# Kernel optimization log

Measured on AMD Instinct MI355X. Metric: run time of the kernel, lower is better.

Reference implementation:

```python
import jax, jax.numpy as jnp
import numpy as np
from jax.scipy.special import logsumexp

T, B, D, L = 1024, 32, 768, 48
NEG = jnp.float32(-1e20)


def setup_inputs() -> dict:
    key = jax.random.key(0)
    ks = jax.random.split(key, 10)
    feats = jax.random.normal(ks[0], (T, B, D), jnp.float32)
    # tags: True = label disallowed at this position (partial annotation mask)
    tags = jax.random.uniform(ks[1], (T, B, L)) < 0.3
    lens = jax.random.randint(ks[2], (B,), T // 2, T + 1)
    W = jax.random.normal(ks[3], (D, L), jnp.float32) * 0.02
    b = jnp.zeros((L,), jnp.float32)
    base = jnp.float32(1.0 / L)
    begin_transition = jnp.full((L,), base) + 0.01 * jax.random.normal(ks[4], (L,), jnp.float32)
    transitions = jnp.full((L, L), base) + 0.01 * jax.random.normal(ks[5], (L, L), jnp.float32)
    end_transition = jnp.full((L,), base) + 0.01 * jax.random.normal(ks[6], (L,), jnp.float32)
    begin_constraints = jax.random.uniform(ks[7], (L,)) < 0.2
    end_constraints = jax.random.uniform(ks[8], (L,)) < 0.2
    transition_constraints = jax.random.uniform(ks[9], (L, L)) < 0.2
    return {
        "feats": feats, "tags": tags, "lens": lens,
        "W": W, "b": b,
        "begin_transition": begin_transition, "transitions": transitions,
        "end_transition": end_transition,
        "begin_constraints": begin_constraints, "end_constraints": end_constraints,
        "transition_constraints": transition_constraints,
    }


def _crf_logZ(emissions, begin, trans, end, tag_mask, lens):
    """Forward algorithm over [T,B,L] emissions; tag_mask True = disallowed.
    Returns log partition per batch element, read out at step lens-1."""
    fs0 = emissions[0] + begin[None, :]              # [B, L]
    fs0 = jnp.where(tag_mask[0], NEG, fs0)

    def step(prev, xs):
        em_t, m_t = xs
        # new[b, j] = logsumexp_k(prev[b, k] + trans[j, k]) + em_t[b, j]
        new = logsumexp(prev[:, None, :] + trans[None, :, :], axis=-1) + em_t
        new = jnp.where(m_t, NEG, new)
        return new, new

    _, ys = jax.lax.scan(step, fs0, (emissions[1:], tag_mask[1:]))
    all_fs = jnp.concatenate([fs0[None], ys], axis=0)        # [T, B, L]
    last = all_fs[lens - 1, jnp.arange(lens.shape[0])]       # [B, L]
    return logsumexp(last + end[None, :], axis=-1)           # [B]


def reference(feats, tags, lens, W, b, begin_transition, transitions,
              end_transition, begin_constraints, end_constraints,
              transition_constraints):
    # feature2labels (Dropout is identity in eval)
    emissions = jnp.einsum('tbd,dl->tbl', feats, W) + b      # [T, B, L]
    no_mask = jnp.zeros_like(tags)

    # forward_alg: unconstrained partition function
    fwd = _crf_logZ(emissions, begin_transition, transitions,
                    end_transition, no_mask, lens)

    # partial_score: constrained params + gold tag masking
    begin_m = jnp.where(begin_constraints, NEG, begin_transition)
    trans_m = jnp.where(transition_constraints, NEG, transitions)
    end_m = jnp.where(end_constraints, NEG, end_transition)
    par = _crf_logZ(emissions, begin_m, trans_m, end_m, tags, lens)

    # criterion per batch element (sum over batch = original scalar loss)
    return fwd - par                                          # [B]
```

## Files before the change

kernel.cpp:

```cpp
#include <hip/hip_runtime.h>

#define T_ 1024
#define B_ 32
#define D_ 768
#define L_ 48
#define TB_ (T_ * B_)

typedef __attribute__((ext_vector_type(4))) float f32x4;

__global__ __launch_bounds__(256, 2) void emis_gemm(
    const float* __restrict__ feats, const float* __restrict__ W,
    const float* __restrict__ bias, float* __restrict__ E) {
  __shared__ float fbuf[64 * 64];
  __shared__ float wbuf[48 * 68];
  const int tid = threadIdx.x;
  const int wv = tid >> 6;
  const int lane = tid & 63;
  const int cg = tid & 7;
  const int rg = tid >> 3;
  const int c0 = cg * 6;
  const int rowbase = blockIdx.x * 64;
  const int r7 = rg & 7;
  const int r_in = lane >> 4;
  const int slot = lane & 15;

  float acc[2][6];
#pragma unroll
  for (int i = 0; i < 2; i++)
#pragma unroll
    for (int c = 0; c < 6; c++) acc[i][c] = 0.f;

  for (int kc = 0; kc < D_; kc += 64) {
    __syncthreads();

#pragma unroll
    for (int inst = 0; inst < 4; inst++) {
      const int rowstart = wv * 16 + inst * 4;
      const int r = rowstart + r_in;
      const int gch = slot ^ (r & 7);
      const float* g = feats + (size_t)(rowbase + r) * D_ + kc + gch * 4;
      float* l = fbuf + rowstart * 64;
      __builtin_amdgcn_global_load_lds(
          (const __attribute__((address_space(1))) uint32_t*)g,
          (__attribute__((address_space(3))) uint32_t*)l, 16, 0, 0);
    }

#pragma unroll
    for (int i = 0; i < 12; i++) {
      const int idx = tid + i * 256;
      const int ko = idx / 48;
      const int j = idx - ko * 48;
      wbuf[j * 68 + ko] = W[(kc + ko) * L_ + j];
    }

    __syncthreads();

#pragma unroll 4
    for (int k4 = 0; k4 < 16; k4++) {
      float4 fv[2];
      float4 wv4[6];
      const int sch = (k4 ^ r7) << 2;
#pragma unroll
      for (int i = 0; i < 2; i++)
        fv[i] = *(const float4*)(fbuf + (rg + 32 * i) * 64 + sch);
#pragma unroll
      for (int cc = 0; cc < 6; cc++)
        wv4[cc] = *(const float4*)(wbuf + (c0 + cc) * 68 + k4 * 4);
#pragma unroll
      for (int i = 0; i < 2; i++) {
#pragma unroll
        for (int cc = 0; cc < 6; cc++) {
          acc[i][cc] = fmaf(fv[i].x, wv4[cc].x, acc[i][cc]);
          acc[i][cc] = fmaf(fv[i].y, wv4[cc].y, acc[i][cc]);
          acc[i][cc] = fmaf(fv[i].z, wv4[cc].z, acc[i][cc]);
          acc[i][cc] = fmaf(fv[i].w, wv4[cc].w, acc[i][cc]);
        }
      }
    }
  }

#pragma unroll
  for (int i = 0; i < 2; i++) {
    float* dst = E + (size_t)(rowbase + rg + 32 * i) * L_ + c0;
#pragma unroll
    for (int cc = 0; cc < 6; cc += 2) {
      float2 v;
      v.x = __expf(acc[i][cc + 0] + bias[c0 + cc + 0]);
      v.y = __expf(acc[i][cc + 1] + bias[c0 + cc + 1]);
      *(float2*)(dst + cc) = v;
    }
  }
}

__global__ __launch_bounds__(128) void crf_scan(
    const float* __restrict__ E, const int* __restrict__ tags,
    const int* __restrict__ lens, const float* __restrict__ begin,
    const float* __restrict__ trans, const float* __restrict__ endt,
    const int* __restrict__ bc, const int* __restrict__ ec,
    const int* __restrict__ tc, float* __restrict__ out) {
  __shared__ __align__(16) float sbuf[2][2][64];
  __shared__ __align__(16) float pbuf[2][48 * 52];
  __shared__ float lzbuf[2];
  const int b = blockIdx.x;
  const int wv = threadIdx.x >> 6;
  const int lane = threadIdx.x & 63;
  const bool act = lane < L_;
  const bool par = (wv == 1);
  const int len = lens[b];
  const int stride = B_ * L_;
  const int base = b * L_ + (act ? lane : 0);

  if (act) {
#pragma unroll
    for (int k = 0; k < L_; k++) {
      float v = __expf(trans[lane * L_ + k]);
      if (par && tc[lane * L_ + k]) v = 0.f;
      pbuf[wv][lane * 52 + k] = v;
    }
  }
  const f32x4* prow = (const f32x4*)(pbuf[wv] + (act ? lane : 0) * 52);

  float a = 0.f;
  if (act) {
    a = E[base] * __expf(begin[lane]);
    if (par && (bc[lane] || tags[base])) a = 0.f;
  }
  float logacc = 0.f;

  sbuf[wv][0][lane] = a;

  auto step = [&](int i, float ev, int tg, bool resc) {
    const f32x4* src = (const f32x4*)sbuf[wv][i & 1];
    float s0 = 0.f, s1 = 0.f, s2 = 0.f, s3 = 0.f;
    f32x4 mx = {0.f, 0.f, 0.f, 0.f};
#pragma unroll
    for (int c = 0; c < 12; c++) {
      const f32x4 pq = prow[c];
      const f32x4 q = src[c];
      if (resc) {
        mx.x = fmaxf(mx.x, q.x);
        mx.y = fmaxf(mx.y, q.y);
        mx.z = fmaxf(mx.z, q.z);
        mx.w = fmaxf(mx.w, q.w);
      }
      s0 = fmaf(q.x, pq.x, s0);
      s1 = fmaf(q.y, pq.y, s1);
      s2 = fmaf(q.z, pq.z, s2);
      s3 = fmaf(q.w, pq.w, s3);
    }
    float evp = ev;
    if (resc) {
      float m = fmaxf(fmaxf(mx.x, mx.y), fmaxf(mx.z, mx.w));
      m = fmaxf(m, 1e-30f);
      logacc += __logf(m);
      evp = ev * (1.f / m);
    }
    float u = ((s0 + s1) + (s2 + s3)) * evp;
    if (tg) u = 0.f;
    a = u;
    sbuf[wv][(i + 1) & 1][lane] = u;
  };

  float e4[4];
  int tg4[4];
#pragma unroll
  for (int i = 0; i < 4; i++) {
    e4[i] = E[(size_t)(1 + i) * stride + base];
    tg4[i] = par ? tags[(size_t)(1 + i) * stride + base] : 0;
  }

  int t = 1;
  for (; t + 4 <= len; t += 4) {
    float p4[4];
    int q4[4];
#pragma unroll
    for (int i = 0; i < 4; i++) {
      int tt = t + 4 + i;
      tt = (tt < len) ? tt : (len - 1);
      p4[i] = E[(size_t)tt * stride + base];
      q4[i] = par ? tags[(size_t)tt * stride + base] : 0;
    }
    if ((t & 7) == 1) {
      step(0, e4[0], tg4[0], true);
    } else {
      step(0, e4[0], tg4[0], false);
    }
    step(1, e4[1], tg4[1], false);
    step(2, e4[2], tg4[2], false);
    step(3, e4[3], tg4[3], false);
#pragma unroll
    for (int i = 0; i < 4; i++) { e4[i] = p4[i]; tg4[i] = q4[i]; }
  }
#pragma unroll
  for (int i = 0; i < 4; i++) {
    if (t + i < len) step(i, e4[i], tg4[i], false);
  }

  float z = 0.f;
  if (act) {
    float ez = __expf(endt[lane]);
    if (par && ec[lane]) ez = 0.f;
    z = a * ez;
  }
#pragma unroll
  for (int off = 32; off; off >>= 1) z += __shfl_xor(z, off, 64);
  if (lane == 0) lzbuf[wv] = logacc + __logf(z);
  __syncthreads();
  if (threadIdx.x == 0) out[b] = lzbuf[0] - lzbuf[1];
}

extern "C" void kernel_launch(void* const* d_in, const int* in_sizes, int n_in,
                              void* d_out, int out_size, void* d_ws,
                              size_t ws_size, hipStream_t stream) {
  (void)in_sizes; (void)n_in; (void)out_size; (void)ws_size;
  const float* feats = (const float*)d_in[0];
  const int* tags = (const int*)d_in[1];
  const int* lens = (const int*)d_in[2];
  const float* W = (const float*)d_in[3];
  const float* bias = (const float*)d_in[4];
  const float* begin = (const float*)d_in[5];
  const float* trans = (const float*)d_in[6];
  const float* endt = (const float*)d_in[7];
  const int* bc = (const int*)d_in[8];
  const int* ec = (const int*)d_in[9];
  const int* tc = (const int*)d_in[10];

  float* E = (float*)d_ws;
  float* out = (float*)d_out;

  emis_gemm<<<dim3(TB_ / 64), dim3(256), 0, stream>>>(feats, W, bias, E);
  crf_scan<<<dim3(B_), dim3(128), 0, stream>>>(E, tags, lens, begin, trans,
                                               endt, bc, ec, tc, out);
}
```

Baseline: 462.4 us.

## Split CRF passes into separate single-wave blocks with transitions in registers

```diff
diff --git a/kernel.cpp b/kernel.cpp
--- a/kernel.cpp
+++ b/kernel.cpp
@@ -92,33 +92,35 @@
   }
 }
 
-__global__ __launch_bounds__(128) void crf_scan(
+__global__ __launch_bounds__(64)
+__attribute__((amdgpu_waves_per_eu(1))) void crf_scan(
     const float* __restrict__ E, const int* __restrict__ tags,
     const int* __restrict__ lens, const float* __restrict__ begin,
     const float* __restrict__ trans, const float* __restrict__ endt,
     const int* __restrict__ bc, const int* __restrict__ ec,
     const int* __restrict__ tc, float* __restrict__ out) {
-  __shared__ __align__(16) float sbuf[2][2][64];
-  __shared__ __align__(16) float pbuf[2][48 * 52];
-  __shared__ float lzbuf[2];
-  const int b = blockIdx.x;
-  const int wv = threadIdx.x >> 6;
-  const int lane = threadIdx.x & 63;
+  __shared__ __align__(16) float sbuf[2][64];
+  const int s = blockIdx.x;
+  const int pass = s & 1;
+  const int b = s >> 1;
+  const int lane = threadIdx.x;
   const bool act = lane < L_;
-  const bool par = (wv == 1);
+  const bool par = (pass == 1);
   const int len = lens[b];
   const int stride = B_ * L_;
   const int base = b * L_ + (act ? lane : 0);
 
+  float P[L_];
+#pragma unroll
+  for (int k = 0; k < L_; k++) P[k] = 0.f;
   if (act) {
 #pragma unroll
     for (int k = 0; k < L_; k++) {
       float v = __expf(trans[lane * L_ + k]);
       if (par && tc[lane * L_ + k]) v = 0.f;
-      pbuf[wv][lane * 52 + k] = v;
-    }
-  }
-  const f32x4* prow = (const f32x4*)(pbuf[wv] + (act ? lane : 0) * 52);
+      P[k] = v;
+    }
+  }
 
   float a = 0.f;
   if (act) {
@@ -127,15 +129,14 @@
   }
   float logacc = 0.f;
 
-  sbuf[wv][0][lane] = a;
+  sbuf[0][lane] = a;
 
   auto step = [&](int i, float ev, int tg, bool resc) {
-    const f32x4* src = (const f32x4*)sbuf[wv][i & 1];
+    const f32x4* src = (const f32x4*)sbuf[i & 1];
     float s0 = 0.f, s1 = 0.f, s2 = 0.f, s3 = 0.f;
     f32x4 mx = {0.f, 0.f, 0.f, 0.f};
 #pragma unroll
     for (int c = 0; c < 12; c++) {
-      const f32x4 pq = prow[c];
       const f32x4 q = src[c];
       if (resc) {
         mx.x = fmaxf(mx.x, q.x);
@@ -143,10 +144,10 @@
         mx.z = fmaxf(mx.z, q.z);
         mx.w = fmaxf(mx.w, q.w);
       }
-      s0 = fmaf(q.x, pq.x, s0);
-      s1 = fmaf(q.y, pq.y, s1);
-      s2 = fmaf(q.z, pq.z, s2);
-      s3 = fmaf(q.w, pq.w, s3);
+      s0 = fmaf(q.x, P[4 * c + 0], s0);
+      s1 = fmaf(q.y, P[4 * c + 1], s1);
+      s2 = fmaf(q.z, P[4 * c + 2], s2);
+      s3 = fmaf(q.w, P[4 * c + 3], s3);
     }
     float evp = ev;
     if (resc) {
@@ -158,7 +159,7 @@
     float u = ((s0 + s1) + (s2 + s3)) * evp;
     if (tg) u = 0.f;
     a = u;
-    sbuf[wv][(i + 1) & 1][lane] = u;
+    sbuf[(i + 1) & 1][lane] = u;
   };
 
   float e4[4];
@@ -204,9 +205,8 @@
   }
 #pragma unroll
   for (int off = 32; off; off >>= 1) z += __shfl_xor(z, off, 64);
-  if (lane == 0) lzbuf[wv] = logacc + __logf(z);
-  __syncthreads();
-  if (threadIdx.x == 0) out[b] = lzbuf[0] - lzbuf[1];
+  const float logZ = logacc + __logf(z);
+  if (lane == 0) atomicAdd(out + b, par ? -logZ : logZ);
 }
 
 extern "C" void kernel_launch(void* const* d_in, const int* in_sizes, int n_in,
@@ -228,7 +228,9 @@
   float* E = (float*)d_ws;
   float* out = (float*)d_out;
 
+  hipMemsetAsync(d_out, 0, B_ * sizeof(float), stream);
+
   emis_gemm<<<dim3(TB_ / 64), dim3(256), 0, stream>>>(feats, W, bias, E);
-  crf_scan<<<dim3(B_), dim3(128), 0, stream>>>(E, tags, lens, begin, trans,
-                                               endt, bc, ec, tc, out);
+  crf_scan<<<dim3(2 * B_), dim3(64), 0, stream>>>(E, tags, lens, begin, trans,
+                                                  endt, bc, ec, tc, out);
 }
```

Result: faster. 425.7 us (-7.9%).
